# Kernel tuning notes

Measured on AMD Instinct MI355X. Metric: run time of the kernel, lower is better.

## Reference

```python
import jax, jax.numpy as jnp
import numpy as np

OH = 512
OW = 512
SCALES = (1, 2, 4)
MAX_RAY = 100
N_POINTS = 2_000_000


def setup_inputs() -> dict:
    key = jax.random.key(0)
    k1, k2, k3 = jax.random.split(key, 3)
    coords = jax.random.uniform(k1, (N_POINTS, 2), jnp.float32)   # normalized screen coords in [0,1)
    depth = jax.random.uniform(k2, (N_POINTS,), jnp.float32)      # raw z depth
    pts_meta = jax.random.normal(k3, (N_POINTS,), jnp.float32)    # per-point payload scattered into rays
    return {"coords": coords, "depth": depth, "pts_meta": pts_meta}


def reference(coords, depth, pts_meta):
    """JAX translation of ForwardSamplerMultiscale3d.forward.

    Torch version produces ragged outputs sized by the (data-dependent) number of
    occupied cells n_cells <= H*W per scale. For jit-compatibility we pad each
    per-scale output along the cell axis to the static maximum HW = (H//s)*(W//s):
      batch:        [MAX_RAY, HW]  (columns >= n_cells are zero)
      rays_lengths: [HW]           (entries >= n_cells are zero)
      canvas_index: [HW, 2]        (rows >= n_cells are zero)
    Occupied cells appear first (sorted by linear cell id), identical math otherwise.
    """
    n = coords.shape[0]
    h0 = OH // SCALES[0]
    w0 = OW // SCALES[0]
    hw = jnp.array([h0, w0], coords.dtype)
    # scale to pixel coords, clamp, floor -> integer cell coords (as in torch)
    c = jnp.floor(jnp.clip(coords * hw, 0.0, hw - 1.0)).astype(jnp.int32)  # [N,2]
    # global sort by depth (ascending, stable)
    order = jnp.argsort(depth)
    c = c[order]
    pm = pts_meta[order]

    ar = jnp.arange(n, dtype=jnp.int32)
    ones_i = jnp.ones((n,), jnp.int32)
    batches, lengths, canvases = [], [], []
    for scale in SCALES:
        h = h0 // scale
        w = w0 // scale
        HW = h * w
        cs = jnp.clip(c // scale, 0, jnp.array([h - 1, w - 1], jnp.int32))  # [N,2]
        cell = cs[:, 0] * w + cs[:, 1]                                      # linear cell id
        # stable sort by cell id preserves depth order within each cell
        ord2 = jnp.argsort(cell)  # jnp.argsort is stable
        cell_s = cell[ord2]
        pm_s = pm[ord2]
        ij = cs[ord2]
        # segment boundaries (new-cell mask)
        change = jnp.concatenate([jnp.ones((1,), bool), cell_s[1:] != cell_s[:-1]])
        seg = jnp.cumsum(change.astype(jnp.int32)) - 1                      # segment id per point
        # start index of each segment -> per-point index within its ray
        starts = jax.ops.segment_min(ar, seg, num_segments=HW)
        idx_in_grp = ar - starts[seg]
        # ray lengths, clamped to MAX_RAY
        lens = jnp.minimum(
            jax.ops.segment_sum(ones_i, seg, num_segments=HW), MAX_RAY
        )
        # (i,j) canvas coordinate of each occupied cell
        canvas = jnp.zeros((HW, 2), jnp.int32).at[seg].set(ij)
        # scatter point payloads into [MAX_RAY, HW] ray buffer; drop overflow
        mask = idx_in_grp < MAX_RAY
        batch = jnp.zeros((MAX_RAY, HW), pm.dtype).at[
            jnp.minimum(idx_in_grp, MAX_RAY - 1), seg
        ].add(jnp.where(mask, pm_s, 0.0))
        batches.append(batch)
        lengths.append(lens)
        canvases.append(canvas)
    return (*batches, *lengths, *canvases)
```

## Files before the change

### kernel.cpp

```cpp
#include <hip/hip_runtime.h>
#include <stdint.h>

#define MAX_RAY 100
#define NBUCK 512
#define PTS_PER_BLK 4096
#define PLACE_CAP 5120
#define CAPB 5120
typedef unsigned long long ull;
typedef uint32_t u32;

#define N0 262144
#define NBLK0 128
#define NBLKB 168
#define LKELEMS 272

__device__ __forceinline__ u32 spread1(u32 v) {
    v &= 0x1FF;
    v = (v | (v << 8)) & 0x00FF00FF;
    v = (v | (v << 4)) & 0x0F0F0F0F;
    v = (v | (v << 2)) & 0x33333333;
    v = (v | (v << 1)) & 0x55555555;
    return v;
}
__device__ __forceinline__ u32 morton2(u32 i, u32 j) { return (spread1(i) << 1) | spread1(j); }

__device__ __forceinline__ void px_of(const float2 cv, int& pi, int& pj) {
    float fi = fminf(fmaxf(cv.x * 512.0f, 0.0f), 511.0f);
    float fj = fminf(fmaxf(cv.y * 512.0f, 0.0f), 511.0f);
    pi = (int)fi;
    pj = (int)fj;
}

__global__ __launch_bounds__(256)
void bucket_hist_kernel(const float2* __restrict__ coords,
                        u32* __restrict__ bucketCnt, int n) {
    __shared__ u32 lh[NBUCK];
    int t = threadIdx.x;
    for (int i = t; i < NBUCK; i += 256) lh[i] = 0;
    __syncthreads();
    int base = blockIdx.x * PTS_PER_BLK;
#pragma unroll
    for (int k = 0; k < 16; ++k) {
        int p = base + k * 256 + t;
        if (p < n) {
            int pi, pj; px_of(coords[p], pi, pj);
            atomicAdd(&lh[morton2(pi, pj) >> 9], 1u);
        }
    }
    __syncthreads();
    for (int i = t; i < NBUCK; i += 256)
        if (lh[i]) atomicAdd(&bucketCnt[i], lh[i]);
}

__global__ __launch_bounds__(NBUCK)
void bucket_scan_kernel(const u32* __restrict__ bucketCnt,
                        u32* __restrict__ bucketStart,
                        u32* __restrict__ bucketCur, int n) {
    __shared__ u32 part[NBUCK];
    int t = threadIdx.x;
    u32 v = bucketCnt[t];
    part[t] = v; __syncthreads();
    for (int off = 1; off < NBUCK; off <<= 1) {
        u32 x = part[t]; u32 a = (t >= off) ? part[t - off] : 0u;
        __syncthreads(); part[t] = x + a; __syncthreads();
    }
    u32 ex = part[t] - v;
    bucketStart[t] = ex; bucketCur[t] = ex;
    if (t == NBUCK - 1) bucketStart[NBUCK] = (u32)n;
}

__global__ __launch_bounds__(256)
void bucket_scatter_kernel(const float2* __restrict__ coords,
                           const float* __restrict__ depth,
                           const float* __restrict__ pm,
                           u32* __restrict__ bucketCur,
                           ull* __restrict__ keys,
                           u32* __restrict__ payg,
                           int n) {
    __shared__ u32 lhist[NBUCK], lofs[NBUCK], lcur[NBUCK], gbase[NBUCK], temp[256];
    __shared__ ull stage[PTS_PER_BLK];
    int t = threadIdx.x;
    for (int i = t; i < NBUCK; i += 256) lhist[i] = 0;
    __syncthreads();
    int base = blockIdx.x * PTS_PER_BLK;
    ull ent[16]; u32 cb[16]; u32 pos[16];
#pragma unroll
    for (int k = 0; k < 16; ++k) {
        int p = base + k * 256 + t;
        cb[k] = 0xFFFFFFFFu;
        if (p < n) {
            int pi, pj; px_of(coords[p], pi, pj);
            u32 m = morton2(pi, pj);
            cb[k] = m >> 9;
            ent[k] = ((ull)__float_as_uint(depth[p]) << 32)
                   | ((ull)(m & 511u) << 21) | (ull)(u32)p;
            atomicAdd(&lhist[cb[k]], 1u);
        }
    }
    __syncthreads();
    u32 pv = lhist[2 * t] + lhist[2 * t + 1];
    temp[t] = pv; __syncthreads();
    for (int off = 1; off < 256; off <<= 1) {
        u32 x = temp[t]; u32 a = (t >= off) ? temp[t - off] : 0u;
        __syncthreads(); temp[t] = x + a; __syncthreads();
    }
    u32 pb = temp[t] - pv;
    lofs[2 * t] = pb;                  lofs[2 * t + 1] = pb + lhist[2 * t];
    lcur[2 * t] = pb;                  lcur[2 * t + 1] = pb + lhist[2 * t];
    __syncthreads();
#pragma unroll
    for (int k = 0; k < 16; ++k) {
        if (cb[k] != 0xFFFFFFFFu) {
            pos[k] = atomicAdd(&lcur[cb[k]], 1u);
            stage[pos[k]] = ent[k];
        }
    }
    __syncthreads();
    for (int b = t; b < NBUCK; b += 256) {
        u32 cnt = lhist[b];
        if (!cnt) continue;
        u32 gb = atomicAdd(&bucketCur[b], cnt);
        gbase[b] = gb;
        u32 lo = lofs[b];
        for (u32 i = 0; i < cnt; ++i) keys[gb + i] = stage[lo + i];
    }
    if (payg) {
        __syncthreads();
        u32* pstage = (u32*)stage;
#pragma unroll
        for (int k = 0; k < 16; ++k) {
            int p = base + k * 256 + t;
            if (cb[k] != 0xFFFFFFFFu) pstage[pos[k]] = __float_as_uint(pm[p]);
        }
        __syncthreads();
        for (int b = t; b < NBUCK; b += 256) {
            u32 cnt = lhist[b];
            if (!cnt) continue;
            u32 gb = gbase[b], lo = lofs[b];
            for (u32 i = 0; i < cnt; ++i) payg[gb + i] = pstage[lo + i];
        }
    }
}

__global__ __launch_bounds__(256)
void cell_hist_kernel(const ull* __restrict__ keys,
                      const u32* __restrict__ bucketStart,
                      u32* __restrict__ countsM) {
    __shared__ u32 lh[NBUCK];
    int b = blockIdx.x, t = threadIdx.x;
    for (int i = t; i < NBUCK; i += 256) lh[i] = 0;
    __syncthreads();
    u32 s = bucketStart[b], e = bucketStart[b + 1];
    for (u32 i = s + t; i < e; i += 256) {
        u32 mlow = (u32)(keys[i] >> 21) & 511u;
        atomicAdd(&lh[mlow], 1u);
    }
    __syncthreads();
    for (int i = t; i < NBUCK; i += 256) countsM[(b << 9) + i] = lh[i];
}

__global__ __launch_bounds__(256)
void place_kernel(ull* __restrict__ keys,
                  u32* __restrict__ payg,
                  const u32* __restrict__ bucketStart,
                  const u32* __restrict__ startsM) {
    __shared__ ull stage[PLACE_CAP];
    __shared__ u32 pstage[PLACE_CAP];
    __shared__ u32 cur[NBUCK];
    int b = blockIdx.x, t = threadIdx.x;
    u32 s = bucketStart[b], e = bucketStart[b + 1];
    u32 cnt = e - s;
    u32 lim = cnt < PLACE_CAP ? cnt : PLACE_CAP;
    for (u32 i = t; i < lim; i += 256) stage[i] = keys[s + i];
    if (payg) for (u32 i = t; i < lim; i += 256) pstage[i] = payg[s + i];
    for (int i = t; i < NBUCK; i += 256) cur[i] = startsM[(b << 9) + i];
    __syncthreads();
    for (u32 i = t; i < lim; i += 256) {
        ull en = stage[i];
        u32 mlow = (u32)(en >> 21) & 511u;
        u32 slot = atomicAdd(&cur[mlow], 1u);
        keys[slot] = ((en >> 32) << 32) | (en & 0x1FFFFFull);
        if (payg) payg[slot] = pstage[i];
    }
}

__global__ __launch_bounds__(256)
void bucket_scatter_fixed(const float2* __restrict__ coords,
                          const float* __restrict__ depth,
                          const float* __restrict__ pm,
                          u32* __restrict__ bucketCnt,
                          ull* __restrict__ stageK,
                          u32* __restrict__ stageP,
                          int n) {
    __shared__ u32 lhist[NBUCK], lofs[NBUCK], lcur[NBUCK], gbase[NBUCK], temp[256];
    __shared__ ull stage[PTS_PER_BLK];
    int t = threadIdx.x;
    for (int i = t; i < NBUCK; i += 256) lhist[i] = 0;
    __syncthreads();
    int base = blockIdx.x * PTS_PER_BLK;
    ull ent[16]; u32 cb[16]; u32 pos[16];
#pragma unroll
    for (int k = 0; k < 16; ++k) {
        int p = base + k * 256 + t;
        cb[k] = 0xFFFFFFFFu;
        if (p < n) {
            int pi, pj; px_of(coords[p], pi, pj);
            u32 m = morton2(pi, pj);
            cb[k] = m >> 9;
            ent[k] = ((ull)__float_as_uint(depth[p]) << 32)
                   | ((ull)(m & 511u) << 21) | (ull)(u32)p;
            atomicAdd(&lhist[cb[k]], 1u);
        }
    }
    __syncthreads();
    u32 pv = lhist[2 * t] + lhist[2 * t + 1];
    temp[t] = pv; __syncthreads();
    for (int off = 1; off < 256; off <<= 1) {
        u32 x = temp[t]; u32 a = (t >= off) ? temp[t - off] : 0u;
        __syncthreads(); temp[t] = x + a; __syncthreads();
    }
    u32 pb = temp[t] - pv;
    lofs[2 * t] = pb;                  lofs[2 * t + 1] = pb + lhist[2 * t];
    lcur[2 * t] = pb;                  lcur[2 * t + 1] = pb + lhist[2 * t];
    __syncthreads();
#pragma unroll
    for (int k = 0; k < 16; ++k) {
        if (cb[k] != 0xFFFFFFFFu) {
            pos[k] = atomicAdd(&lcur[cb[k]], 1u);
            stage[pos[k]] = ent[k];
        }
    }
    __syncthreads();
    for (int b = t; b < NBUCK; b += 256) {
        u32 cnt = lhist[b];
        if (!cnt) { gbase[b] = 0xFFFFFFFFu; continue; }
        u32 gb0 = atomicAdd(&bucketCnt[b], cnt);
        gbase[b] = gb0;
        u32 wr = (gb0 >= CAPB) ? 0u : ((cnt < CAPB - gb0) ? cnt : CAPB - gb0);
        u32 gb = b * CAPB + gb0, lo = lofs[b];
        for (u32 i = 0; i < wr; ++i) stageK[gb + i] = stage[lo + i];
    }
    __syncthreads();
    u32* pstage = (u32*)stage;
#pragma unroll
    for (int k = 0; k < 16; ++k) {
        int p = base + k * 256 + t;
        if (cb[k] != 0xFFFFFFFFu) pstage[pos[k]] = __float_as_uint(pm[p]);
    }
    __syncthreads();
    for (int b = t; b < NBUCK; b += 256) {
        u32 cnt = lhist[b], gb0 = gbase[b];
        if (!cnt || gb0 == 0xFFFFFFFFu) continue;
        u32 wr = (gb0 >= CAPB) ? 0u : ((cnt < CAPB - gb0) ? cnt : CAPB - gb0);
        u32 gb = b * CAPB + gb0, lo = lofs[b];
        for (u32 i = 0; i < wr; ++i) stageP[gb + i] = pstage[lo + i];
    }
}

__global__ __launch_bounds__(NBUCK)
void bucket_scan2(const u32* __restrict__ bucketCnt,
                  u32* __restrict__ bucketStart) {
    __shared__ u32 part[NBUCK];
    int t = threadIdx.x;
    u32 v = bucketCnt[t]; if (v > CAPB) v = CAPB;
    part[t] = v; __syncthreads();
    for (int off = 1; off < NBUCK; off <<= 1) {
        u32 x = part[t]; u32 a = (t >= off) ? part[t - off] : 0u;
        __syncthreads(); part[t] = x + a; __syncthreads();
    }
    bucketStart[t] = part[t] - v;
    if (t == NBUCK - 1) bucketStart[NBUCK] = part[t];
}

__global__ __launch_bounds__(256)
void cell_hist_staged(const ull* __restrict__ stageK,
                      const u32* __restrict__ bucketCnt,
                      u32* __restrict__ countsM) {
    __shared__ u32 lh[NBUCK];
    int b = blockIdx.x, t = threadIdx.x;
    for (int i = t; i < NBUCK; i += 256) lh[i] = 0;
    __syncthreads();
    u32 cnt = bucketCnt[b]; if (cnt > CAPB) cnt = CAPB;
    u32 s = (u32)b * CAPB;
    for (u32 i = t; i < cnt; i += 256) {
        u32 mlow = (u32)(stageK[s + i] >> 21) & 511u;
        atomicAdd(&lh[mlow], 1u);
    }
    __syncthreads();
    for (int i = t; i < NBUCK; i += 256) countsM[(b << 9) + i] = lh[i];
}

__global__ __launch_bounds__(256)
void place_staged(const ull* __restrict__ stageK,
                  const u32* __restrict__ stageP,
                  const u32* __restrict__ bucketCnt,
                  const u32* __restrict__ startsM,
                  ull* __restrict__ keysF,
                  u32* __restrict__ payF) {
    __shared__ u32 cur[NBUCK];
    int b = blockIdx.x, t = threadIdx.x;
    u32 cnt = bucketCnt[b]; if (cnt > CAPB) cnt = CAPB;
    for (int i = t; i < NBUCK; i += 256) cur[i] = startsM[(b << 9) + i];
    __syncthreads();
    u32 s = (u32)b * CAPB;
    for (u32 i = t; i < cnt; i += 256) {
        ull en = stageK[s + i];
        u32 mlow = (u32)(en >> 21) & 511u;
        u32 slot = atomicAdd(&cur[mlow], 1u);
        keysF[slot] = ((en >> 32) << 32) | (en & 0x1FFFFFull);
        payF[slot] = stageP[s + i];
    }
}

__global__ __launch_bounds__(256)
void scanA_final2(const u32* __restrict__ countsM,
                  const u32* __restrict__ bucketStart,
                  u32* __restrict__ startsM) {
    int b = blockIdx.x, t = threadIdx.x;
    const uint4* src = (const uint4*)(countsM + b * 2048);
    uint4 a = src[t * 2], c = src[t * 2 + 1];
    u32 e[8] = {a.x, a.y, a.z, a.w, c.x, c.y, c.z, c.w};
    u32 tsum = 0;
#pragma unroll
    for (int k = 0; k < 8; ++k) tsum += e[k];
    __shared__ u32 part[256];
    part[t] = tsum; __syncthreads();
    for (int off = 1; off < 256; off <<= 1) {
        u32 x = part[t];
        u32 ad = (t >= off) ? part[t - off] : 0;
        __syncthreads(); part[t] = x + ad; __syncthreads();
    }
    u32 run = bucketStart[b * 4] + part[t] - tsum;
    u32 o[8];
#pragma unroll
    for (int k = 0; k < 8; ++k) { o[k] = run; run += e[k]; }
    uint4* d1 = (uint4*)(startsM + b * 2048);
    d1[t * 2]     = make_uint4(o[0], o[1], o[2], o[3]);
    d1[t * 2 + 1] = make_uint4(o[4], o[5], o[6], o[7]);
    if (b == NBLK0 - 1 && t == 255) startsM[N0] = run;
}

__device__ __forceinline__ void blk_map(int b, int& si, int& bb) {
    if (b < 128)      { si = 0; bb = b; }
    else if (b < 160) { si = 1; bb = b - 128; }
    else              { si = 2; bb = b - 160; }
}
__device__ __forceinline__ u32 cell_cnt(const u32* startsM, int c, int wbits, int si) {
    u32 ci = (u32)c >> wbits, cj = (u32)c & ((1u << wbits) - 1u);
    u32 mb = morton2(ci, cj) << (2 * si);
    return startsM[mb + (1u << (2 * si))] - startsM[mb];
}

__global__ __launch_bounds__(256)
void scanB_partial(const u32* __restrict__ startsM, u32* __restrict__ bsumB) {
    int si, bb; blk_map(blockIdx.x, si, bb);
    int wbits = 9 - si, t = threadIdx.x;
    int base = bb * 2048 + t * 8;
    u32 s = 0;
#pragma unroll
    for (int k = 0; k < 8; ++k)
        s += (cell_cnt(startsM, base + k, wbits, si) > 0) ? 1u : 0u;
    __shared__ u32 red[256];
    red[t] = s; __syncthreads();
    for (int off = 128; off; off >>= 1) {
        if (t < off) red[t] += red[t + off];
        __syncthreads();
    }
    if (!t) bsumB[blockIdx.x] = red[0];
}

__global__ __launch_bounds__(256)
void scanB_bsum(const u32* __restrict__ bsumB, u32* __restrict__ bpreB,
                u32* __restrict__ ncells) {
    __shared__ u32 part[256];
    int t = threadIdx.x;
    u32 v = (t < NBLKB) ? bsumB[t] : 0u;
    int rid = (t < 128) ? 0 : ((t < 160) ? 1 : 2);
    part[t] = v; __syncthreads();
    for (int off = 1; off < 256; off <<= 1) {
        u32 x = part[t];
        int tp = t - off;
        int ridp = (tp < 128) ? 0 : ((tp < 160) ? 1 : 2);
        u32 a = (tp >= 0 && ridp == rid) ? part[tp] : 0u;
        __syncthreads(); part[t] = x + a; __syncthreads();
    }
    if (t < NBLKB) bpreB[t] = part[t] - v;
    if (t == 127) ncells[0] = part[t];
    if (t == 159) ncells[1] = part[t];
    if (t == 167) ncells[2] = part[t];
}

struct SegArgs {
    u32* segid[3]; float* lens[3]; float* canvas[3];
};
__global__ __launch_bounds__(256)
void scanB_final(const u32* __restrict__ startsM, const u32* __restrict__ bpreB,
                 SegArgs sa) {
    int si, bb; blk_map(blockIdx.x, si, bb);
    int wbits = 9 - si, t = threadIdx.x;
    int base = bb * 2048 + t * 8;
    u32 cnt[8], flg[8], tsum = 0;
#pragma unroll
    for (int k = 0; k < 8; ++k) {
        cnt[k] = cell_cnt(startsM, base + k, wbits, si);
        flg[k] = cnt[k] ? 1u : 0u;
        tsum += flg[k];
    }
    __shared__ u32 part[256];
    part[t] = tsum; __syncthreads();
    for (int off = 1; off < 256; off <<= 1) {
        u32 x = part[t];
        u32 ad = (t >= off) ? part[t - off] : 0u;
        __syncthreads(); part[t] = x + ad; __syncthreads();
    }
    u32 run = bpreB[blockIdx.x] + part[t] - tsum;
    u32* segid = sa.segid[si];
    float* lens = sa.lens[si];
    float* canvas = sa.canvas[si];
    u32 wmask = (1u << wbits) - 1u;
#pragma unroll
    for (int k = 0; k < 8; ++k) {
        int c = base + k;
        segid[c] = run;
        if (flg[k]) {
            u32 s = run;
            u32 len = cnt[k] < MAX_RAY ? cnt[k] : MAX_RAY;
            lens[s] = (float)len;
            canvas[2 * s]     = (float)((u32)c >> wbits);
            canvas[2 * s + 1] = (float)((u32)c & wmask);
            run += 1;
        }
    }
}

struct CellRegs { ull k0, k1, k2, k3; u32 p0, p1, p2, p3; };
struct __attribute__((packed, aligned(8))) U2 { ull x, y; };
struct __attribute__((packed, aligned(4))) U4 { u32 x, y, z, w; };

template<int CAP>
__device__ __forceinline__ void loadCellG(const ull* __restrict__ keys,
                                          const u32* __restrict__ payg,
                                          const float* __restrict__ pm,
                                          u32 s0, u32 cnt, u32 li, CellRegs& c) {
    c.k0 = c.k1 = c.k2 = c.k3 = ~0ull;
    c.p0 = c.p1 = c.p2 = c.p3 = 0u;
    u32 m = li * 4u;
    if (cnt == 0u || cnt > (u32)CAP || m >= cnt) return;
    const U2* kp = (const U2*)(keys + s0 + m);
    U2 a = kp[0], b = kp[1];
    c.k0 = a.x; c.k1 = a.y; c.k2 = b.x; c.k3 = b.y;
    if (payg) {
        U4 pv = *(const U4*)(payg + s0 + m);
        c.p0 = pv.x; c.p1 = pv.y; c.p2 = pv.z; c.p3 = pv.w;
    } else {
        c.p0 = __float_as_uint(pm[(u32)(c.k0 & 0x1FFFFFull)]);
        if (m + 1 < cnt) c.p1 = __float_as_uint(pm[(u32)(c.k1 & 0x1FFFFFull)]);
        if (m + 2 < cnt) c.p2 = __float_as_uint(pm[(u32)(c.k2 & 0x1FFFFFull)]);
        if (m + 3 < cnt) c.p3 = __float_as_uint(pm[(u32)(c.k3 & 0x1FFFFFull)]);
    }
    if (m + 1 >= cnt) c.k1 = ~0ull;
    if (m + 2 >= cnt) c.k2 = ~0ull;
    if (m + 3 >= cnt) c.k3 = ~0ull;
}

template<int SI>
__device__ __forceinline__ void emit_body(
    const float* __restrict__ pm, const u32* __restrict__ payload,
    const u32* __restrict__ startsM, const ull* __restrict__ keys,
    const u32* __restrict__ segid, float* __restrict__ batch, int bb,
    float (&tile)[MAX_RAY][65], ull (&lkAll)[4][LKELEMS],
    u32 (&s_s0)[64], u32 (&s_cnt)[64], u32 (&s_seg)[64],
    u32 (&ovfl)[64], u32& ovflN)
{
    constexpr int WB   = 9 - SI;
    constexpr int G    = (SI == 0) ? 8 : (SI == 1) ? 16 : 64;
    constexpr int CAP  = G * 4;
    constexpr int STRD = (SI == 0) ? 34 : (SI == 1) ? 66 : 256;
    constexpr int NG   = 64 / G;
    constexpr int ROUNDS = 64 / (4 * NG);
    const int HW = 1 << (2 * WB);

    int t = threadIdx.x, wave = t >> 6, lane = t & 63;
    int gi = lane / G, li = lane % G;
    ull* lk = &lkAll[wave][0];

    if (t == 0) ovflN = 0;
    if (t < 64) {
        int cell = bb * 64 + t;
        u32 ci = (u32)cell >> WB, cj = (u32)cell & ((1u << WB) - 1u);
        u32 mb = morton2(ci, cj) << (2 * SI);
        u32 s0 = startsM[mb];
        s_s0[t]  = s0;
        s_cnt[t] = startsM[mb + (1u << (2 * SI))] - s0;
        s_seg[t] = segid[cell];
    }
    __syncthreads();

    CellRegs cur, nxt;
    {
        int lc0 = wave * NG + gi;
        loadCellG<CAP>(keys, payload, pm, s_s0[lc0], s_cnt[lc0], (u32)li, cur);
    }
#pragma unroll
    for (int rnd = 0; rnd < ROUNDS; ++rnd) {
        int lc = (rnd * 4 + wave) * NG + gi;
        u32 cnt = s_cnt[lc], m = (u32)li * 4u;
        bool fits = (cnt <= (u32)CAP);
        if (fits && m < cnt) {
            ull* dst = lk + gi * STRD + m;
            dst[0] = cur.k0; dst[1] = cur.k1; dst[2] = cur.k2; dst[3] = cur.k3;
        }
        if (!fits && li == 0) {
            u32 ix = atomicAdd(&ovflN, 1u);
            ovfl[ix] = (u32)lc;
        }
        if (rnd + 1 < ROUNDS) {
            int lc2 = ((rnd + 1) * 4 + wave) * NG + gi;
            loadCellG<CAP>(keys, payload, pm, s_s0[lc2], s_cnt[lc2], (u32)li, nxt);
        }
        if (cnt && fits) {
            asm volatile("s_waitcnt lgkmcnt(0)" ::: "memory");
            u32 cntR = (cnt + 3u) & ~3u;
            u32 r0 = 0, r1 = 0, r2 = 0, r3 = 0;
            const ull* kb = lk + gi * STRD;
            for (u32 j = 0; j < cntR; j += 4) {
                U2 a  = *(const U2*)(kb + j);
                U2 b2 = *(const U2*)(kb + j + 2);
                r0 += (a.x < cur.k0) + (a.y < cur.k0) + (b2.x < cur.k0) + (b2.y < cur.k0);
                r1 += (a.x < cur.k1) + (a.y < cur.k1) + (b2.x < cur.k1) + (b2.y < cur.k1);
                r2 += (a.x < cur.k2) + (a.y < cur.k2) + (b2.x < cur.k2) + (b2.y < cur.k2);
                r3 += (a.x < cur.k3) + (a.y < cur.k3) + (b2.x < cur.k3) + (b2.y < cur.k3);
            }
            if (m < cnt) {
                if (r0 < MAX_RAY)                 tile[r0][lc] = __uint_as_float(cur.p0);
                if (m + 1 < cnt && r1 < MAX_RAY)  tile[r1][lc] = __uint_as_float(cur.p1);
                if (m + 2 < cnt && r2 < MAX_RAY)  tile[r2][lc] = __uint_as_float(cur.p2);
                if (m + 3 < cnt && r3 < MAX_RAY)  tile[r3][lc] = __uint_as_float(cur.p3);
            }
        }
        cur = nxt;
    }
    __syncthreads();

    u32 no = ovflN;
    if (no && wave == 0) {
        for (u32 o = 0; o < no; ++o) {
            int lc = (int)ovfl[o];
            u32 s0 = s_s0[lc], cnt = s_cnt[lc];
            for (u32 i = lane; i < cnt; i += 64) {
                ull mk = keys[s0 + i];
                u32 r = 0;
                for (u32 j = 0; j < cnt; ++j) r += (keys[s0 + j] < mk) ? 1u : 0u;
                if (r < MAX_RAY) {
                    u32 pv = payload ? payload[s0 + i]
                                     : __float_as_uint(pm[(u32)(mk & 0x1FFFFFull)]);
                    tile[r][lc] = __uint_as_float(pv);
                }
            }
        }
    }
    __syncthreads();

    u32 myCnt = s_cnt[lane], mySeg = s_seg[lane];
    u32 lim = myCnt < MAX_RAY ? myCnt : MAX_RAY;
    for (int r = wave; r < MAX_RAY; r += 4) {
        if (myCnt) batch[(size_t)r * (size_t)HW + mySeg] = (r < (int)lim) ? tile[r][lane] : 0.0f;
    }
}

struct EmitArgs {
    const u32* segid[3]; float* batch[3];
};
__global__ __launch_bounds__(256)
void emit_kernel(const float* __restrict__ pm,
                 const u32* __restrict__ payload,
                 const u32* __restrict__ startsM,
                 const ull* __restrict__ keys,
                 EmitArgs ea) {
    __shared__ float tile[MAX_RAY][65];
    __shared__ __align__(16) ull lkAll[4][LKELEMS];
    __shared__ u32 s_s0[64], s_cnt[64], s_seg[64], ovfl[64], ovflN;

    int b = blockIdx.x;
    if (b < 256)
        emit_body<2>(pm, payload, startsM, keys, ea.segid[2], ea.batch[2], b,
                     tile, lkAll, s_s0, s_cnt, s_seg, ovfl, ovflN);
    else if (b < 1280)
        emit_body<1>(pm, payload, startsM, keys, ea.segid[1], ea.batch[1], b - 256,
                     tile, lkAll, s_s0, s_cnt, s_seg, ovfl, ovflN);
    else
        emit_body<0>(pm, payload, startsM, keys, ea.segid[0], ea.batch[0], b - 1280,
                     tile, lkAll, s_s0, s_cnt, s_seg, ovfl, ovflN);
}

__global__ __launch_bounds__(256)
void zero_tail_kernel(const u32* __restrict__ ncells,
                      float* __restrict__ b0, float* __restrict__ b1,
                      float* __restrict__ b2,
                      float* __restrict__ l0, float* __restrict__ l1,
                      float* __restrict__ l2,
                      float* __restrict__ c0, float* __restrict__ c1,
                      float* __restrict__ c2) {
    int b = blockIdx.x, si, col; float* base; float* lens; float* canv; int HW;
    if (b < 1024)      { si = 0; base = b0; lens = l0; canv = c0; HW = 262144; col = b * 256 + (int)threadIdx.x; }
    else if (b < 1280) { si = 1; base = b1; lens = l1; canv = c1; HW = 65536;  col = (b - 1024) * 256 + (int)threadIdx.x; }
    else               { si = 2; base = b2; lens = l2; canv = c2; HW = 16384;  col = (b - 1280) * 256 + (int)threadIdx.x; }
    if ((u32)col >= ncells[si]) {
        lens[col] = 0.0f;
        canv[2 * col] = 0.0f; canv[2 * col + 1] = 0.0f;
        for (int r = 0; r < MAX_RAY; ++r)
            base[(size_t)r * (size_t)HW + col] = 0.0f;
    }
}

extern "C" void kernel_launch(void* const* d_in, const int* in_sizes, int n_in,
                              void* d_out, int out_size, void* d_ws, size_t ws_size,
                              hipStream_t stream) {
    const float2* coords = (const float2*)d_in[0];
    const float*  depth  = (const float*)d_in[1];
    const float*  pm     = (const float*)d_in[2];
    float* out = (float*)d_out;
    const int n = in_sizes[1];

    const int HWs[3] = {512 * 512, 256 * 256, 128 * 128};

    char* ws = (char*)d_ws;
    size_t off = 0;
    ull* keysF   = (ull*)(ws + off); off += (size_t)n * 8;
    u32* countsM = (u32*)(ws + off); off += (size_t)N0 * 4;
    u32* startsM = (u32*)(ws + off); off += (size_t)(N0 + 64) * 4;
    u32* segid[3];
    for (int i = 0; i < 3; ++i) { segid[i] = (u32*)(ws + off); off += (size_t)HWs[i] * 4; }
    u32* bsumB = (u32*)(ws + off); off += 256 * 4;
    u32* bpreB = (u32*)(ws + off); off += 256 * 4;
    u32* bucketCnt   = (u32*)(ws + off); off += NBUCK * 4;
    u32* bucketStart = (u32*)(ws + off); off += (NBUCK + 64) * 4;
    u32* bucketCur   = (u32*)(ws + off); off += NBUCK * 4;
    u32* ncells      = (u32*)(ws + off); off += 64 * 4;
    u32* payF        = (u32*)(ws + off);
    size_t needPay = off + (size_t)n * 4;
    size_t offStage = needPay;
    ull* stageK = (ull*)(ws + offStage);
    u32* stageP = (u32*)(ws + offStage + (size_t)NBUCK * CAPB * 8);
    size_t needStaged = offStage + (size_t)NBUCK * CAPB * 12;

    bool haveStage = (ws_size >= needStaged);
    u32* payg = (ws_size >= needPay) ? payF : nullptr;

    size_t offB[3], offL[3], offC[3];
    size_t o = 0;
    for (int i = 0; i < 3; ++i) { offB[i] = o; o += (size_t)MAX_RAY * HWs[i]; }
    for (int i = 0; i < 3; ++i) { offL[i] = o; o += (size_t)HWs[i]; }
    for (int i = 0; i < 3; ++i) { offC[i] = o; o += 2 * (size_t)HWs[i]; }

    hipMemsetAsync(bucketCnt, 0, NBUCK * 4, stream);

    const int nblkPts = (n + PTS_PER_BLK - 1) / PTS_PER_BLK;

    if (haveStage) {
        bucket_scatter_fixed<<<nblkPts, 256, 0, stream>>>(coords, depth, pm, bucketCnt,
                                                          stageK, stageP, n);
        bucket_scan2<<<1, NBUCK, 0, stream>>>(bucketCnt, bucketStart);
        cell_hist_staged<<<NBUCK, 256, 0, stream>>>(stageK, bucketCnt, countsM);
        scanA_final2<<<NBLK0, 256, 0, stream>>>(countsM, bucketStart, startsM);
        place_staged<<<NBUCK, 256, 0, stream>>>(stageK, stageP, bucketCnt, startsM,
                                                keysF, payF);
        payg = payF;
    } else {
        bucket_hist_kernel<<<nblkPts, 256, 0, stream>>>(coords, bucketCnt, n);
        bucket_scan_kernel<<<1, NBUCK, 0, stream>>>(bucketCnt, bucketStart, bucketCur, n);
        bucket_scatter_kernel<<<nblkPts, 256, 0, stream>>>(coords, depth, pm, bucketCur,
                                                           keysF, payg, n);
        cell_hist_kernel<<<NBUCK, 256, 0, stream>>>(keysF, bucketStart, countsM);
        scanA_final2<<<NBLK0, 256, 0, stream>>>(countsM, bucketStart, startsM);
        place_kernel<<<NBUCK, 256, 0, stream>>>(keysF, payg, bucketStart, startsM);
    }

    SegArgs sa;
    for (int i = 0; i < 3; ++i) {
        sa.segid[i]  = segid[i];
        sa.lens[i]   = out + offL[i];
        sa.canvas[i] = out + offC[i];
    }
    scanB_partial<<<NBLKB, 256, 0, stream>>>(startsM, bsumB);
    scanB_bsum<<<1, 256, 0, stream>>>(bsumB, bpreB, ncells);
    scanB_final<<<NBLKB, 256, 0, stream>>>(startsM, bpreB, sa);

    EmitArgs ea;
    for (int i = 0; i < 3; ++i) {
        ea.segid[i] = segid[i];
        ea.batch[i] = out + offB[i];
    }
    emit_kernel<<<5376, 256, 0, stream>>>(pm, payg, startsM, keysF, ea);
    zero_tail_kernel<<<1344, 256, 0, stream>>>(ncells,
        out + offB[0], out + offB[1], out + offB[2],
        out + offL[0], out + offL[1], out + offL[2],
        out + offC[0], out + offC[1], out + offC[2]);
}
```

Baseline: 188.3 us.

## Fuse cell histogram, scan and placement into one kernel; drop block-sum scan launch

Merges cell_hist_staged, scanA_final2 and place_staged into a single per-bucket kernel that builds the histogram in shared memory, scans it locally and places keys, so the countsM round trip and two launches go away. scanB_bsum is removed: each scanB_final block now sums the preceding block totals itself and writes ncells. The emit tile is also transposed to [64][101] to change the shared-memory access pattern. The cost is some redundant prefix summing per block and different LDS bank behaviour in emit.

```diff
diff --git a/kernel.cpp b/kernel.cpp
--- a/kernel.cpp
+++ b/kernel.cpp
@@ -157,6 +157,34 @@
     }
     __syncthreads();
     for (int i = t; i < NBUCK; i += 256) countsM[(b << 9) + i] = lh[i];
+}
+
+__global__ __launch_bounds__(256)
+void scanA_final2(const u32* __restrict__ countsM,
+                  const u32* __restrict__ bucketStart,
+                  u32* __restrict__ startsM) {
+    int b = blockIdx.x, t = threadIdx.x;
+    const uint4* src = (const uint4*)(countsM + b * 2048);
+    uint4 a = src[t * 2], c = src[t * 2 + 1];
+    u32 e[8] = {a.x, a.y, a.z, a.w, c.x, c.y, c.z, c.w};
+    u32 tsum = 0;
+#pragma unroll
+    for (int k = 0; k < 8; ++k) tsum += e[k];
+    __shared__ u32 part[256];
+    part[t] = tsum; __syncthreads();
+    for (int off = 1; off < 256; off <<= 1) {
+        u32 x = part[t];
+        u32 ad = (t >= off) ? part[t - off] : 0;
+        __syncthreads(); part[t] = x + ad; __syncthreads();
+    }
+    u32 run = bucketStart[b * 4] + part[t] - tsum;
+    u32 o[8];
+#pragma unroll
+    for (int k = 0; k < 8; ++k) { o[k] = run; run += e[k]; }
+    uint4* d1 = (uint4*)(startsM + b * 2048);
+    d1[t * 2]     = make_uint4(o[0], o[1], o[2], o[3]);
+    d1[t * 2 + 1] = make_uint4(o[4], o[5], o[6], o[7]);
+    if (b == NBLK0 - 1 && t == 255) startsM[N0] = run;
 }
 
 __global__ __launch_bounds__(256)
@@ -259,7 +287,8 @@
 
 __global__ __launch_bounds__(NBUCK)
 void bucket_scan2(const u32* __restrict__ bucketCnt,
-                  u32* __restrict__ bucketStart) {
+                  u32* __restrict__ bucketStart,
+                  u32* __restrict__ startsM) {
     __shared__ u32 part[NBUCK];
     int t = threadIdx.x;
     u32 v = bucketCnt[t]; if (v > CAPB) v = CAPB;
@@ -269,40 +298,41 @@
         __syncthreads(); part[t] = x + a; __syncthreads();
     }
     bucketStart[t] = part[t] - v;
-    if (t == NBUCK - 1) bucketStart[NBUCK] = part[t];
-}
-
-__global__ __launch_bounds__(256)
-void cell_hist_staged(const ull* __restrict__ stageK,
-                      const u32* __restrict__ bucketCnt,
-                      u32* __restrict__ countsM) {
-    __shared__ u32 lh[NBUCK];
+    if (t == NBUCK - 1) { bucketStart[NBUCK] = part[t]; startsM[N0] = part[t]; }
+}
+
+__global__ __launch_bounds__(256)
+void place_fused(const ull* __restrict__ stageK,
+                 const u32* __restrict__ stageP,
+                 const u32* __restrict__ bucketCnt,
+                 const u32* __restrict__ bucketStart,
+                 u32* __restrict__ startsM,
+                 ull* __restrict__ keysF,
+                 u32* __restrict__ payF) {
+    __shared__ u32 lh[NBUCK], cur[NBUCK], temp[256];
     int b = blockIdx.x, t = threadIdx.x;
-    for (int i = t; i < NBUCK; i += 256) lh[i] = 0;
-    __syncthreads();
     u32 cnt = bucketCnt[b]; if (cnt > CAPB) cnt = CAPB;
     u32 s = (u32)b * CAPB;
+    for (int i = t; i < NBUCK; i += 256) lh[i] = 0;
+    __syncthreads();
     for (u32 i = t; i < cnt; i += 256) {
         u32 mlow = (u32)(stageK[s + i] >> 21) & 511u;
         atomicAdd(&lh[mlow], 1u);
     }
     __syncthreads();
-    for (int i = t; i < NBUCK; i += 256) countsM[(b << 9) + i] = lh[i];
-}
-
-__global__ __launch_bounds__(256)
-void place_staged(const ull* __restrict__ stageK,
-                  const u32* __restrict__ stageP,
-                  const u32* __restrict__ bucketCnt,
-                  const u32* __restrict__ startsM,
-                  ull* __restrict__ keysF,
-                  u32* __restrict__ payF) {
-    __shared__ u32 cur[NBUCK];
-    int b = blockIdx.x, t = threadIdx.x;
-    u32 cnt = bucketCnt[b]; if (cnt > CAPB) cnt = CAPB;
-    for (int i = t; i < NBUCK; i += 256) cur[i] = startsM[(b << 9) + i];
-    __syncthreads();
-    u32 s = (u32)b * CAPB;
+    u32 bs = bucketStart[b];
+    u32 pv = lh[2 * t] + lh[2 * t + 1];
+    temp[t] = pv; __syncthreads();
+    for (int off = 1; off < 256; off <<= 1) {
+        u32 x = temp[t]; u32 a = (t >= off) ? temp[t - off] : 0u;
+        __syncthreads(); temp[t] = x + a; __syncthreads();
+    }
+    u32 pb = temp[t] - pv;
+    u32 st0 = bs + pb, st1 = bs + pb + lh[2 * t];
+    cur[2 * t] = st0; cur[2 * t + 1] = st1;
+    uint2* d = (uint2*)(startsM + (b << 9));
+    d[t] = make_uint2(st0, st1);
+    __syncthreads();
     for (u32 i = t; i < cnt; i += 256) {
         ull en = stageK[s + i];
         u32 mlow = (u32)(en >> 21) & 511u;
@@ -310,34 +340,6 @@
         keysF[slot] = ((en >> 32) << 32) | (en & 0x1FFFFFull);
         payF[slot] = stageP[s + i];
     }
-}
-
-__global__ __launch_bounds__(256)
-void scanA_final2(const u32* __restrict__ countsM,
-                  const u32* __restrict__ bucketStart,
-                  u32* __restrict__ startsM) {
-    int b = blockIdx.x, t = threadIdx.x;
-    const uint4* src = (const uint4*)(countsM + b * 2048);
-    uint4 a = src[t * 2], c = src[t * 2 + 1];
-    u32 e[8] = {a.x, a.y, a.z, a.w, c.x, c.y, c.z, c.w};
-    u32 tsum = 0;
-#pragma unroll
-    for (int k = 0; k < 8; ++k) tsum += e[k];
-    __shared__ u32 part[256];
-    part[t] = tsum; __syncthreads();
-    for (int off = 1; off < 256; off <<= 1) {
-        u32 x = part[t];
-        u32 ad = (t >= off) ? part[t - off] : 0;
-        __syncthreads(); part[t] = x + ad; __syncthreads();
-    }
-    u32 run = bucketStart[b * 4] + part[t] - tsum;
-    u32 o[8];
-#pragma unroll
-    for (int k = 0; k < 8; ++k) { o[k] = run; run += e[k]; }
-    uint4* d1 = (uint4*)(startsM + b * 2048);
-    d1[t * 2]     = make_uint4(o[0], o[1], o[2], o[3]);
-    d1[t * 2 + 1] = make_uint4(o[4], o[5], o[6], o[7]);
-    if (b == NBLK0 - 1 && t == 255) startsM[N0] = run;
 }
 
 __device__ __forceinline__ void blk_map(int b, int& si, int& bb) {
@@ -369,35 +371,22 @@
     if (!t) bsumB[blockIdx.x] = red[0];
 }
 
-__global__ __launch_bounds__(256)
-void scanB_bsum(const u32* __restrict__ bsumB, u32* __restrict__ bpreB,
-                u32* __restrict__ ncells) {
-    __shared__ u32 part[256];
-    int t = threadIdx.x;
-    u32 v = (t < NBLKB) ? bsumB[t] : 0u;
-    int rid = (t < 128) ? 0 : ((t < 160) ? 1 : 2);
-    part[t] = v; __syncthreads();
-    for (int off = 1; off < 256; off <<= 1) {
-        u32 x = part[t];
-        int tp = t - off;
-        int ridp = (tp < 128) ? 0 : ((tp < 160) ? 1 : 2);
-        u32 a = (tp >= 0 && ridp == rid) ? part[tp] : 0u;
-        __syncthreads(); part[t] = x + a; __syncthreads();
-    }
-    if (t < NBLKB) bpreB[t] = part[t] - v;
-    if (t == 127) ncells[0] = part[t];
-    if (t == 159) ncells[1] = part[t];
-    if (t == 167) ncells[2] = part[t];
-}
-
 struct SegArgs {
     u32* segid[3]; float* lens[3]; float* canvas[3];
 };
 __global__ __launch_bounds__(256)
-void scanB_final(const u32* __restrict__ startsM, const u32* __restrict__ bpreB,
-                 SegArgs sa) {
+void scanB_final(const u32* __restrict__ startsM, const u32* __restrict__ bsumB,
+                 SegArgs sa, u32* __restrict__ ncells) {
     int si, bb; blk_map(blockIdx.x, si, bb);
     int wbits = 9 - si, t = threadIdx.x;
+    int segStart = (si == 0) ? 0 : (si == 1) ? 128 : 160;
+    __shared__ u32 s_bpre;
+    if (t < 64) {
+        u32 acc = 0;
+        for (int j = segStart + t; j < (int)blockIdx.x; j += 64) acc += bsumB[j];
+        for (int o = 32; o; o >>= 1) acc += __shfl_down(acc, o);
+        if (t == 0) s_bpre = acc;
+    }
     int base = bb * 2048 + t * 8;
     u32 cnt[8], flg[8], tsum = 0;
 #pragma unroll
@@ -413,7 +402,7 @@
         u32 ad = (t >= off) ? part[t - off] : 0u;
         __syncthreads(); part[t] = x + ad; __syncthreads();
     }
-    u32 run = bpreB[blockIdx.x] + part[t] - tsum;
+    u32 run = s_bpre + part[t] - tsum;
     u32* segid = sa.segid[si];
     float* lens = sa.lens[si];
     float* canvas = sa.canvas[si];
@@ -431,6 +420,8 @@
             run += 1;
         }
     }
+    if (t == 255 && (blockIdx.x == 127 || blockIdx.x == 159 || blockIdx.x == 167))
+        ncells[si] = run;
 }
 
 struct CellRegs { ull k0, k1, k2, k3; u32 p0, p1, p2, p3; };
@@ -468,7 +459,7 @@
     const float* __restrict__ pm, const u32* __restrict__ payload,
     const u32* __restrict__ startsM, const ull* __restrict__ keys,
     const u32* __restrict__ segid, float* __restrict__ batch, int bb,
-    float (&tile)[MAX_RAY][65], ull (&lkAll)[4][LKELEMS],
+    float (&tile)[64][101], ull (&lkAll)[4][LKELEMS],
     u32 (&s_s0)[64], u32 (&s_cnt)[64], u32 (&s_seg)[64],
     u32 (&ovfl)[64], u32& ovflN)
 {
@@ -532,10 +523,10 @@
                 r3 += (a.x < cur.k3) + (a.y < cur.k3) + (b2.x < cur.k3) + (b2.y < cur.k3);
             }
             if (m < cnt) {
-                if (r0 < MAX_RAY)                 tile[r0][lc] = __uint_as_float(cur.p0);
-                if (m + 1 < cnt && r1 < MAX_RAY)  tile[r1][lc] = __uint_as_float(cur.p1);
-                if (m + 2 < cnt && r2 < MAX_RAY)  tile[r2][lc] = __uint_as_float(cur.p2);
-                if (m + 3 < cnt && r3 < MAX_RAY)  tile[r3][lc] = __uint_as_float(cur.p3);
+                if (r0 < MAX_RAY)                 tile[lc][r0] = __uint_as_float(cur.p0);
+                if (m + 1 < cnt && r1 < MAX_RAY)  tile[lc][r1] = __uint_as_float(cur.p1);
+                if (m + 2 < cnt && r2 < MAX_RAY)  tile[lc][r2] = __uint_as_float(cur.p2);
+                if (m + 3 < cnt && r3 < MAX_RAY)  tile[lc][r3] = __uint_as_float(cur.p3);
             }
         }
         cur = nxt;
@@ -554,7 +545,7 @@
                 if (r < MAX_RAY) {
                     u32 pv = payload ? payload[s0 + i]
                                      : __float_as_uint(pm[(u32)(mk & 0x1FFFFFull)]);
-                    tile[r][lc] = __uint_as_float(pv);
+                    tile[lc][r] = __uint_as_float(pv);
                 }
             }
         }
@@ -564,7 +555,7 @@
     u32 myCnt = s_cnt[lane], mySeg = s_seg[lane];
     u32 lim = myCnt < MAX_RAY ? myCnt : MAX_RAY;
     for (int r = wave; r < MAX_RAY; r += 4) {
-        if (myCnt) batch[(size_t)r * (size_t)HW + mySeg] = (r < (int)lim) ? tile[r][lane] : 0.0f;
+        if (myCnt) batch[(size_t)r * (size_t)HW + mySeg] = (r < (int)lim) ? tile[lane][r] : 0.0f;
     }
 }
 
@@ -577,7 +568,7 @@
                  const u32* __restrict__ startsM,
                  const ull* __restrict__ keys,
                  EmitArgs ea) {
-    __shared__ float tile[MAX_RAY][65];
+    __shared__ float tile[64][101];
     __shared__ __align__(16) ull lkAll[4][LKELEMS];
     __shared__ u32 s_s0[64], s_cnt[64], s_seg[64], ovfl[64], ovflN;
 
@@ -632,7 +623,6 @@
     u32* segid[3];
     for (int i = 0; i < 3; ++i) { segid[i] = (u32*)(ws + off); off += (size_t)HWs[i] * 4; }
     u32* bsumB = (u32*)(ws + off); off += 256 * 4;
-    u32* bpreB = (u32*)(ws + off); off += 256 * 4;
     u32* bucketCnt   = (u32*)(ws + off); off += NBUCK * 4;
     u32* bucketStart = (u32*)(ws + off); off += (NBUCK + 64) * 4;
     u32* bucketCur   = (u32*)(ws + off); off += NBUCK * 4;
@@ -660,11 +650,9 @@
     if (haveStage) {
         bucket_scatter_fixed<<<nblkPts, 256, 0, stream>>>(coords, depth, pm, bucketCnt,
                                                           stageK, stageP, n);
-        bucket_scan2<<<1, NBUCK, 0, stream>>>(bucketCnt, bucketStart);
-        cell_hist_staged<<<NBUCK, 256, 0, stream>>>(stageK, bucketCnt, countsM);
-        scanA_final2<<<NBLK0, 256, 0, stream>>>(countsM, bucketStart, startsM);
-        place_staged<<<NBUCK, 256, 0, stream>>>(stageK, stageP, bucketCnt, startsM,
-                                                keysF, payF);
+        bucket_scan2<<<1, NBUCK, 0, stream>>>(bucketCnt, bucketStart, startsM);
+        place_fused<<<NBUCK, 256, 0, stream>>>(stageK, stageP, bucketCnt, bucketStart,
+                                               startsM, keysF, payF);
         payg = payF;
     } else {
         bucket_hist_kernel<<<nblkPts, 256, 0, stream>>>(coords, bucketCnt, n);
@@ -683,8 +671,7 @@
         sa.canvas[i] = out + offC[i];
     }
     scanB_partial<<<NBLKB, 256, 0, stream>>>(startsM, bsumB);
-    scanB_bsum<<<1, 256, 0, stream>>>(bsumB, bpreB, ncells);
-    scanB_final<<<NBLKB, 256, 0, stream>>>(startsM, bpreB, sa);
+    scanB_final<<<NBLKB, 256, 0, stream>>>(startsM, bsumB, sa, ncells);
 
     EmitArgs ea;
     for (int i = 0; i < 3; ++i) {
```

Measured after the change: 178.5 us. 5.2% less time.
